# Kernel tuning notes

Measured on AMD Instinct MI355X. Metric: run time of the kernel, lower is better.

## Reference

```python
import jax, jax.numpy as jnp
import numpy as np

MID = 16
HEADS = 8
HEAD_DIM = MID // HEADS  # 2
EPS = 1e-5


def posembed(length, dim):
    # get_posembed_linear: sin-cos 1D positional embedding
    pos = jnp.arange(length, dtype=jnp.float32)
    omega = jnp.arange(dim // 2, dtype=jnp.float32) / (dim / 2.0)
    omega = 1.0 / (10000.0 ** omega)
    out = pos[:, None] * omega[None, :]  # [L, dim//2]
    return jnp.concatenate([jnp.sin(out), jnp.cos(out)], axis=1)  # [L, dim]


def layernorm(x, g, b):
    m = x.mean(-1, keepdims=True)
    v = ((x - m) ** 2).mean(-1, keepdims=True)
    return (x - m) * jax.lax.rsqrt(v + EPS) * g + b


def conv2d(x, w, b):
    # NCHW 3x3 SAME conv
    y = jax.lax.conv_general_dilated(x, w, (1, 1), 'SAME',
                                     dimension_numbers=('NCHW', 'OIHW', 'NCHW'))
    return y + b[None, :, None, None]


def attention(x, wq, wk, wv, wo, bo):
    # diffusers Attention: self-attn, no qkv bias, out bias
    B, S, C = x.shape
    q = (x @ wq.T).reshape(B, S, HEADS, HEAD_DIM)
    k = (x @ wk.T).reshape(B, S, HEADS, HEAD_DIM)
    v = (x @ wv.T).reshape(B, S, HEADS, HEAD_DIM)
    scale = 1.0 / np.sqrt(HEAD_DIM).astype(np.float32)
    scores = jnp.einsum('bshd,bthd->bhst', q, k) * scale
    p = jax.nn.softmax(scores, axis=-1)
    o = jnp.einsum('bhst,bthd->bshd', p, v).reshape(B, S, C)
    return o @ wo.T + bo


def setup_inputs() -> dict:
    key = jax.random.key(0)
    ks = jax.random.split(key, 24)

    def n(k, shape, s=0.05):
        return jax.random.normal(k, shape, dtype=jnp.float32) * s

    b, f, h, w, c = 2, 16, 64, 64, 16
    inp = {
        'hidden_states': n(ks[0], (b, f, h, w, c), 1.0),
        'ref_stats': n(ks[1], (b, f, h, w, c), 1.0),
        'emb': n(ks[2], (b, 512), 1.0),
        'conv_in_w': n(ks[3], (MID, c, 3, 3)),
        'conv_in_b': jnp.zeros((MID,), jnp.float32),
        'emb1_w': n(ks[4], (MID, 512)),
        'emb1_b': jnp.zeros((MID,), jnp.float32),
        'emb2_w': n(ks[5], (MID, MID)),
        'emb2_b': jnp.zeros((MID,), jnp.float32),
        'wqx': n(ks[6], (MID, MID)), 'wkx': n(ks[7], (MID, MID)),
        'wvx': n(ks[8], (MID, MID)), 'wox': n(ks[9], (MID, MID)),
        'box': jnp.zeros((MID,), jnp.float32),
        'wqy': n(ks[10], (MID, MID)), 'wky': n(ks[11], (MID, MID)),
        'wvy': n(ks[12], (MID, MID)), 'woy': n(ks[13], (MID, MID)),
        'boy': jnp.zeros((MID,), jnp.float32),
        'wqt': n(ks[14], (MID, MID)), 'wkt': n(ks[15], (MID, MID)),
        'wvt': n(ks[16], (MID, MID)), 'wot': n(ks[17], (MID, MID)),
        'bot': jnp.zeros((MID,), jnp.float32),
        'norm_g': jnp.ones((MID,), jnp.float32),
        'norm_b': jnp.zeros((MID,), jnp.float32),
        'proj_w': n(ks[18], (c, MID, 3, 3)),  # zero_module in torch; random here so grads flow
        'proj_b': jnp.zeros((c,), jnp.float32),
    }
    return inp


def reference(hidden_states, ref_stats, emb,
              conv_in_w, conv_in_b, emb1_w, emb1_b, emb2_w, emb2_b,
              wqx, wkx, wvx, wox, box,
              wqy, wky, wvy, woy, boy,
              wqt, wkt, wvt, wot, bot,
              norm_g, norm_b, proj_w, proj_b):
    b, f, h, w, c = hidden_states.shape

    # conv stem on (b f) c h w
    x = hidden_states.reshape(b * f, h, w, c).transpose(0, 3, 1, 2)
    x = conv2d(x, conv_in_w, conv_in_b)
    r = ref_stats.reshape(b * f, h, w, c).transpose(0, 3, 1, 2)
    r = conv2d(r, conv_in_w, conv_in_b)

    # TimestepEmbedding: linear -> silu -> linear, broadcast over frames/HW
    e = jax.nn.silu(emb @ emb1_w.T + emb1_b) @ emb2_w.T + emb2_b  # [b, MID]
    r = r + jnp.repeat(e, f, axis=0)[:, :, None, None]

    hs = x.reshape(b, f, MID, h, w).transpose(0, 1, 3, 4, 2)  # b f h w c
    rs = r.reshape(b, f, MID, h, w).transpose(0, 1, 3, 4, 2)

    # row (x) attention: cat along w -> (b f h) 2w c
    cat = jnp.concatenate([hs, rs], axis=3).reshape(b * f * h, 2 * w, MID)
    pe = posembed(2 * w, MID)
    resx = attention(layernorm(cat + pe[None], norm_g, norm_b), wqx, wkx, wvx, wox, box)
    resx = resx[:, :w].reshape(b, f, h, w, MID)

    # column (y) attention: cat along h -> (b f w) 2h c
    cat = jnp.concatenate([resx, rs], axis=2)            # b f 2h w c
    cat = cat.transpose(0, 1, 3, 2, 4).reshape(b * f * w, 2 * h, MID)
    pe = posembed(2 * h, MID)
    resy = attention(layernorm(cat + pe[None], norm_g, norm_b), wqy, wky, wvy, woy, boy)
    resy = resy[:, :h].reshape(b, f, w, h, MID).transpose(0, 1, 3, 2, 4)

    # temporal (t) attention: cat along f -> (b h w) 2f c
    cat = jnp.concatenate([resy, rs], axis=1)            # b 2f h w c
    cat = cat.transpose(0, 2, 3, 1, 4).reshape(b * h * w, 2 * f, MID)
    pe = posembed(2 * f, MID)
    rest = attention(layernorm(cat + pe[None], norm_g, norm_b), wqt, wkt, wvt, wot, bot)
    rest = rest[:, :f].reshape(b, h, w, f, MID).transpose(0, 3, 4, 1, 2).reshape(b * f, MID, h, w)

    out = conv2d(rest, proj_w, proj_b)  # (b f) c h w
    return hidden_states + out.reshape(b, f, c, h, w).transpose(0, 1, 3, 4, 2)
```

## Files before the change

kernel.cpp:

```cpp
#include <hip/hip_runtime.h>
#include <hip/hip_bf16.h>

typedef __hip_bfloat16 bf16;
using hf2 = decltype(__builtin_amdgcn_cvt_pkrtz(0.f, 0.f));
typedef float f32x2 __attribute__((ext_vector_type(2)));

__device__ __forceinline__ float b2f(bf16 x) { return __bfloat162float(x); }

#define BB   2
#define FF   16
#define HH   64
#define WW   64
#define CC   16
#define NIMG (BB*FF)
#define PIX  (HH*WW)
#define IMGSZ (PIX*CC)

#define QSCALE_LOG2E 1.0201394f

__device__ __forceinline__ unsigned pkh2(float a, float b) {
    union { hf2 h; unsigned u; } x;
    x.h = __builtin_amdgcn_cvt_pkrtz(a, b);
    return x.u;
}
__device__ __forceinline__ float fdot2u(unsigned a, unsigned b, float c) {
    union { unsigned u; hf2 h; } A, B;
    A.u = a; B.u = b;
    return __builtin_amdgcn_fdot2(A.h, B.h, c, false);
}
__device__ __forceinline__ f32x2 f2(float a, float b) {
    f32x2 r; r.x = a; r.y = b; return r;
}

__device__ __forceinline__ void ld16bf(const bf16* p, float* x) {
    const uint4* p4 = reinterpret_cast<const uint4*>(p);
    uint4 u0 = p4[0], u1 = p4[1];
    unsigned uu[8] = {u0.x, u0.y, u0.z, u0.w, u1.x, u1.y, u1.z, u1.w};
    #pragma unroll
    for (int k = 0; k < 8; ++k) {
        union { unsigned u; float f; } lo, hi;
        lo.u = uu[k] << 16;
        hi.u = uu[k] & 0xffff0000u;
        x[2 * k] = lo.f;
        x[2 * k + 1] = hi.f;
    }
}
__device__ __forceinline__ void st16bf(bf16* p, const float* x) {
    union { bf16 h[16]; uint4 u[2]; } o;
    #pragma unroll
    for (int k = 0; k < 16; ++k) o.h[k] = __float2bfloat16(x[k]);
    uint4* p4 = reinterpret_cast<uint4*>(p);
    p4[0] = o.u[0];
    p4[1] = o.u[1];
}

__device__ __forceinline__ void ld16f(const float* p, float* x) {
    const float4* p4 = reinterpret_cast<const float4*>(p);
    #pragma unroll
    for (int q = 0; q < 4; ++q) {
        float4 v = p4[q];
        x[4 * q] = v.x; x[4 * q + 1] = v.y; x[4 * q + 2] = v.z; x[4 * q + 3] = v.w;
    }
}
__device__ __forceinline__ void st16f(float* p, const float* x) {
    float4* p4 = reinterpret_cast<float4*>(p);
    #pragma unroll
    for (int q = 0; q < 4; ++q)
        p4[q] = make_float4(x[4 * q], x[4 * q + 1], x[4 * q + 2], x[4 * q + 3]);
}

__device__ __forceinline__ unsigned packbf2(float a, float b) {
    union { bf16 h[2]; unsigned u; } pk;
    pk.h[0] = __float2bfloat16(a);
    pk.h[1] = __float2bfloat16(b);
    return pk.u;
}

__global__ __launch_bounds__(256) void conv_in_kernel(
    const float* __restrict__ hid, const float* __restrict__ ref,
    const float* __restrict__ cw, const float* __restrict__ cb,
    const float* __restrict__ emb,
    const float* __restrict__ e1w, const float* __restrict__ e1b,
    const float* __restrict__ e2w, const float* __restrict__ e2b,
    bf16* __restrict__ A, bf16* __restrict__ R)
{
    __shared__ unsigned w2l[9 * 128];
    __shared__ float bl[16];
    __shared__ float hl[16];
    __shared__ float el[16];
    int t = threadIdx.x;
    if (t < 128) {
        int oc = t & 15, c2 = t >> 4;
        #pragma unroll
        for (int k = 0; k < 9; ++k)
            w2l[k * 128 + oc * 8 + c2] =
                pkh2(cw[(oc * 16 + 2 * c2) * 9 + k],
                     cw[(oc * 16 + 2 * c2 + 1) * 9 + k]);
    }
    if (t < 16) bl[t] = cb[t];

    int gid  = blockIdx.x * 256 + t;
    int wi   = gid & 63;
    int hi   = (gid >> 6) & 63;
    int img2 = gid >> 12;
    int isref = img2 >> 5;
    int img  = img2 & 31;
    int bi   = img >> 4;

    if (isref) {
        if (t < 16) {
            float acc = e1b[t];
            const float* er = emb + bi * 512;
            const float* wr = e1w + t * 512;
            for (int k = 0; k < 512; ++k) acc = fmaf(er[k], wr[k], acc);
            hl[t] = acc / (1.f + __expf(-acc));
        }
        __syncthreads();
        if (t < 16) {
            float acc = e2b[t];
            #pragma unroll
            for (int k = 0; k < 16; ++k) acc = fmaf(hl[k], e2w[t * 16 + k], acc);
            el[t] = acc;
        }
    }
    __syncthreads();

    const float* inp = (isref ? ref : hid) + (size_t)img * IMGSZ;
    float acc[16];
    #pragma unroll
    for (int oc = 0; oc < 16; ++oc)
        acc[oc] = bl[oc] + (isref ? el[oc] : 0.f);

    for (int ky = 0; ky < 3; ++ky) {
        int y = hi + ky - 1;
        if ((unsigned)y >= 64u) continue;
        for (int kx = 0; kx < 3; ++kx) {
            int x = wi + kx - 1;
            if ((unsigned)x >= 64u) continue;
            float xv[16];
            ld16f(inp + (((y << 6) + x) << 4), xv);
            unsigned xp[8];
            #pragma unroll
            for (int c2 = 0; c2 < 8; ++c2)
                xp[c2] = pkh2(xv[2 * c2], xv[2 * c2 + 1]);
            const unsigned* wt = &w2l[(ky * 3 + kx) * 128];
            #pragma unroll
            for (int oc = 0; oc < 16; ++oc) {
                float a = acc[oc];
                #pragma unroll
                for (int c2 = 0; c2 < 8; ++c2)
                    a = fdot2u(xp[c2], wt[oc * 8 + c2], a);
                acc[oc] = a;
            }
        }
    }
    bf16* op = (isref ? R : A) + ((size_t)(img * PIX + (hi << 6) + wi) << 4);
    st16bf(op, acc);
}

template<int S, int SEQPB, int MINW, bool F16OUT>
__global__ __launch_bounds__(256, MINW) void attn_kernel(
    bf16* __restrict__ A, const bf16* __restrict__ R,
    unsigned* __restrict__ A16,
    int d2, int str1, int str2, int tokStride,
    const float* __restrict__ wq, const float* __restrict__ wk,
    const float* __restrict__ wv, const float* __restrict__ wo,
    const float* __restrict__ bo, const float* __restrict__ gw,
    const float* __restrict__ bw)
{
    constexpr int HS  = S / 2;
    constexpr int KQ  = S / 2;
    constexpr int TPT = 256 / (SEQPB * S);
    constexpr int NDIM = 16 / TPT;
    constexpr int ITEMS = 256 / SEQPB;
    constexpr int NQG = ITEMS / 16;
    constexpr int QB  = HS / NQG;
    constexpr int QP  = QB / 2;
    constexpr int KROW = 10;
    constexpr int QROW = 20;
    constexpr int LSQ = (SEQPB == 1) ? 0 : ((SEQPB == 2) ? 1 : 2);
    constexpr int NW3 = SEQPB * HS * 8 / 256;

    __shared__ float wolT[256];
    __shared__ unsigned wq2L[128], wk2L[128], wv2L[128];
    __shared__ float bol[16], gl[16], blw[16];
    __shared__ __align__(16) unsigned kU[SEQPB * S * KROW];
    __shared__ __align__(16) unsigned vU[SEQPB * S * KROW];
    __shared__ __align__(16) unsigned qL[SEQPB * HS * KROW];
    __shared__ int bases[SEQPB];

    int t = threadIdx.x;
    wolT[(t & 15) * 16 + (t >> 4)] = wo[t];
    if (t < 128) {
        float2 qw = reinterpret_cast<const float2*>(wq)[t];
        float2 kw = reinterpret_cast<const float2*>(wk)[t];
        float2 vw = reinterpret_cast<const float2*>(wv)[t];
        wq2L[t] = pkh2(qw.x * QSCALE_LOG2E, qw.y * QSCALE_LOG2E);
        wk2L[t] = pkh2(kw.x, kw.y);
        wv2L[t] = pkh2(vw.x, vw.y);
    }
    if (t < 16) { bol[t] = bo[t]; gl[t] = gw[t]; blw[t] = bw[t]; }
    if (t < SEQPB) {
        int seq = blockIdx.x * SEQPB + t;
        bases[t] = (seq / d2) * str1 + (seq % d2) * str2;
    }
    __syncthreads();

    {
        int tokIdx = (TPT == 2) ? (t >> 1) : t;
        int db     = (TPT == 2) ? ((t & 1) * 8) : 0;
        int sq = tokIdx & (SEQPB - 1);
        int i  = tokIdx >> LSQ;
        const bf16* src = (i < HS)
            ? (A + bases[sq] + (size_t)i * tokStride)
            : (R + bases[sq] + (size_t)(i - HS) * tokStride);
        float x[16];
        ld16bf(src, x);
        const float om[8] = {1.f, 0.31622776601683794f, 0.1f, 0.031622776601683794f,
                             0.01f, 0.0031622776601683794f, 0.001f, 0.00031622776601683794f};
        float fi = (float)i;
        #pragma unroll
        for (int k = 0; k < 8; ++k) {
            float sv, cv;
            __sincosf(fi * om[k], &sv, &cv);
            x[k]     += sv;
            x[k + 8] += cv;
        }
        float m = 0.f;
        #pragma unroll
        for (int c = 0; c < 16; ++c) m += x[c];
        m *= (1.f / 16.f);
        float var = 0.f;
        #pragma unroll
        for (int c = 0; c < 16; ++c) { float d = x[c] - m; var = fmaf(d, d, var); }
        var *= (1.f / 16.f);
        float rs = rsqrtf(var + 1e-5f);
        float xn[16];
        #pragma unroll
        for (int c = 0; c < 16; ++c) xn[c] = (x[c] - m) * rs * gl[c] + blw[c];

        unsigned xp[8];
        #pragma unroll
        for (int c2 = 0; c2 < 8; ++c2) xp[c2] = pkh2(xn[2 * c2], xn[2 * c2 + 1]);

        float qv[NDIM], kv[NDIM], vv[NDIM];
        #pragma unroll
        for (int dd = 0; dd < NDIM; ++dd) {
            int d = db + dd;
            float aq = 0.f, ak = 0.f, av = 0.f;
            #pragma unroll
            for (int c2 = 0; c2 < 8; ++c2) {
                aq = fdot2u(xp[c2], wq2L[d * 8 + c2], aq);
                ak = fdot2u(xp[c2], wk2L[d * 8 + c2], ak);
                av = fdot2u(xp[c2], wv2L[d * 8 + c2], av);
            }
            qv[dd] = aq; kv[dd] = ak; vv[dd] = av;
        }
        int row = (sq * S + i) * KROW + (db >> 1);
        uint2* kr = reinterpret_cast<uint2*>(&kU[row]);
        uint2* vr = reinterpret_cast<uint2*>(&vU[row]);
        #pragma unroll
        for (int e = 0; e < NDIM / 4; ++e) {
            kr[e] = make_uint2(pkh2(kv[4 * e], kv[4 * e + 1]),
                               pkh2(kv[4 * e + 2], kv[4 * e + 3]));
            vr[e] = make_uint2(packbf2(vv[4 * e], vv[4 * e + 1]),
                               packbf2(vv[4 * e + 2], vv[4 * e + 3]));
        }
        if (i < HS) {
            uint2* qr = reinterpret_cast<uint2*>(&qL[(sq * HS + i) * KROW + (db >> 1)]);
            #pragma unroll
            for (int e = 0; e < NDIM / 4; ++e)
                qr[e] = make_uint2(pkh2(qv[4 * e], qv[4 * e + 1]),
                                   pkh2(qv[4 * e + 2], qv[4 * e + 3]));
        }
    }
    __syncthreads();

    int sq2 = t / ITEMS;
    int r   = t % ITEMS;
    int qg  = r >> 4;
    int hd  = (r >> 1) & 7;
    int half = r & 1;
    float* oL = reinterpret_cast<float*>(kU);
    {
        unsigned q2[QB];
        f32x2 l2[QP], a0p[QP], a1p[QP];
        #pragma unroll
        for (int qq = 0; qq < QB; ++qq)
            q2[qq] = qL[(sq2 * HS + qg * QB + qq) * KROW + hd];
        #pragma unroll
        for (int m = 0; m < QP; ++m) {
            l2[m] = f2(0.f, 0.f); a0p[m] = f2(0.f, 0.f); a1p[m] = f2(0.f, 0.f);
        }
        const unsigned* kp = &kU[(sq2 * S + half) * KROW + hd];
        const unsigned* vp = &vU[(sq2 * S + half) * KROW + hd];
        #pragma unroll 8
        for (int jj = 0; jj < KQ; ++jj) {
            unsigned ku = kp[jj * 2 * KROW];
            unsigned vu = vp[jj * 2 * KROW];
            union { unsigned u; float f; } v0, v1;
            v0.u = vu << 16; v1.u = vu & 0xffff0000u;
            f32x2 v00 = f2(v0.f, v0.f);
            f32x2 v11 = f2(v1.f, v1.f);
            #pragma unroll
            for (int m = 0; m < QP; ++m) {
                f32x2 p2;
                p2.x = __builtin_amdgcn_exp2f(fdot2u(q2[2 * m], ku, 0.f));
                p2.y = __builtin_amdgcn_exp2f(fdot2u(q2[2 * m + 1], ku, 0.f));
                l2[m] += p2;
                a0p[m] = __builtin_elementwise_fma(p2, v00, a0p[m]);
                a1p[m] = __builtin_elementwise_fma(p2, v11, a1p[m]);
            }
        }
        #pragma unroll
        for (int m = 0; m < QP; ++m) {
            l2[m].x  += __shfl_xor(l2[m].x, 1);  l2[m].y  += __shfl_xor(l2[m].y, 1);
            a0p[m].x += __shfl_xor(a0p[m].x, 1); a0p[m].y += __shfl_xor(a0p[m].y, 1);
            a1p[m].x += __shfl_xor(a1p[m].x, 1); a1p[m].y += __shfl_xor(a1p[m].y, 1);
        }
        __syncthreads();
        if (half == 0) {
            #pragma unroll
            for (int m = 0; m < QP; ++m) {
                float inv0 = 1.f / l2[m].x;
                float inv1 = 1.f / l2[m].y;
                *reinterpret_cast<float2*>(
                    &oL[(sq2 * HS + qg * QB + 2 * m) * QROW + 2 * hd]) =
                    make_float2(a0p[m].x * inv0, a1p[m].x * inv0);
                *reinterpret_cast<float2*>(
                    &oL[(sq2 * HS + qg * QB + 2 * m + 1) * QROW + 2 * hd]) =
                    make_float2(a0p[m].y * inv1, a1p[m].y * inv1);
            }
        }
    }
    __syncthreads();

    #pragma unroll
    for (int rep = 0; rep < NW3; ++rep) {
        int idx = t + rep * 256;
        int cp  = idx & 7;
        int g   = idx >> 3;
        int sq3 = g & (SEQPB - 1);
        int tok = g >> LSQ;
        const float* orow = &oL[(sq3 * HS + tok) * QROW];
        float acc0 = bol[2 * cp], acc1 = bol[2 * cp + 1];
        #pragma unroll
        for (int d = 0; d < 16; ++d) {
            acc0 = fmaf(orow[d], wolT[d * 16 + 2 * cp], acc0);
            acc1 = fmaf(orow[d], wolT[d * 16 + 2 * cp + 1], acc1);
        }
        int off = bases[sq3] + tok * tokStride;
        *reinterpret_cast<unsigned*>(A + off + 2 * cp) = packbf2(acc0, acc1);
        if constexpr (F16OUT)
            A16[(off >> 1) + cp] = pkh2(acc0, acc1);
    }
}

__global__ __launch_bounds__(256) void conv_out_kernel(
    const unsigned* __restrict__ A16, const float* __restrict__ hid,
    const float* __restrict__ pw, const float* __restrict__ pb,
    float* __restrict__ out)
{
    __shared__ unsigned w2l[9 * 128];
    __shared__ float bl[16];
    int t = threadIdx.x;
    if (t < 128) {
        int oc = t & 15, c2 = t >> 4;
        #pragma unroll
        for (int k = 0; k < 9; ++k)
            w2l[k * 128 + oc * 8 + c2] =
                pkh2(pw[(oc * 16 + 2 * c2) * 9 + k],
                     pw[(oc * 16 + 2 * c2 + 1) * 9 + k]);
    }
    if (t < 16) bl[t] = pb[t];
    __syncthreads();

    int gid = blockIdx.x * 256 + t;
    int wi = gid & 63, hi = (gid >> 6) & 63;
    int img = gid >> 12;
    const unsigned* inp = A16 + ((size_t)img << 15);
    float acc[16];
    #pragma unroll
    for (int oc = 0; oc < 16; ++oc) acc[oc] = bl[oc];

    for (int ky = 0; ky < 3; ++ky) {
        int y = hi + ky - 1;
        if ((unsigned)y >= 64u) continue;
        for (int kx = 0; kx < 3; ++kx) {
            int x = wi + kx - 1;
            if ((unsigned)x >= 64u) continue;
            const uint4* p4 = reinterpret_cast<const uint4*>(
                inp + (((y << 6) + x) << 3));
            uint4 u0 = p4[0], u1 = p4[1];
            unsigned xp[8] = {u0.x, u0.y, u0.z, u0.w, u1.x, u1.y, u1.z, u1.w};
            const unsigned* wt = &w2l[(ky * 3 + kx) * 128];
            #pragma unroll
            for (int oc = 0; oc < 16; ++oc) {
                float a = acc[oc];
                #pragma unroll
                for (int c2 = 0; c2 < 8; ++c2)
                    a = fdot2u(xp[c2], wt[oc * 8 + c2], a);
                acc[oc] = a;
            }
        }
    }
    size_t off = ((size_t)gid) << 4;
    float hv[16];
    ld16f(hid + off, hv);
    float res[16];
    #pragma unroll
    for (int k = 0; k < 16; ++k) res[k] = acc[k] + hv[k];
    st16f(out + off, res);
}

extern "C" void kernel_launch(void* const* d_in, const int* in_sizes, int n_in,
                              void* d_out, int out_size, void* d_ws, size_t ws_size,
                              hipStream_t stream) {
    const float* hid  = (const float*)d_in[0];
    const float* ref  = (const float*)d_in[1];
    const float* emb  = (const float*)d_in[2];
    const float* ciw  = (const float*)d_in[3];
    const float* cib  = (const float*)d_in[4];
    const float* e1w  = (const float*)d_in[5];
    const float* e1b  = (const float*)d_in[6];
    const float* e2w  = (const float*)d_in[7];
    const float* e2b  = (const float*)d_in[8];
    const float* wqx  = (const float*)d_in[9];
    const float* wkx  = (const float*)d_in[10];
    const float* wvx  = (const float*)d_in[11];
    const float* wox  = (const float*)d_in[12];
    const float* box_ = (const float*)d_in[13];
    const float* wqy  = (const float*)d_in[14];
    const float* wky  = (const float*)d_in[15];
    const float* wvy  = (const float*)d_in[16];
    const float* woy  = (const float*)d_in[17];
    const float* boy  = (const float*)d_in[18];
    const float* wqt  = (const float*)d_in[19];
    const float* wkt  = (const float*)d_in[20];
    const float* wvt  = (const float*)d_in[21];
    const float* wot  = (const float*)d_in[22];
    const float* bot  = (const float*)d_in[23];
    const float* ng   = (const float*)d_in[24];
    const float* nb   = (const float*)d_in[25];
    const float* pjw  = (const float*)d_in[26];
    const float* pjb  = (const float*)d_in[27];

    bf16* A = (bf16*)d_ws;
    unsigned* A16 = (unsigned*)((char*)d_ws + (4 << 20));
    bf16* R = (bf16*)d_out;

    conv_in_kernel<<<(2 * NIMG * PIX) / 256, 256, 0, stream>>>(
        hid, ref, ciw, cib, emb, e1w, e1b, e2w, e2b, A, R);

    attn_kernel<128, 1, 8, false><<<BB * FF * HH, 256, 0, stream>>>(
        A, R, nullptr, 1, WW * CC, 0, CC, wqx, wkx, wvx, wox, box_, ng, nb);
    attn_kernel<128, 2, 4, false><<<(BB * FF * WW) / 2, 256, 0, stream>>>(
        A, R, nullptr, WW, IMGSZ, CC, WW * CC, wqy, wky, wvy, woy, boy, ng, nb);
    attn_kernel<32, 4, 8, true><<<(BB * HH * WW) / 4, 256, 0, stream>>>(
        A, R, A16, HH * WW, FF * IMGSZ, CC, IMGSZ, wqt, wkt, wvt, wot, bot, ng, nb);

    conv_out_kernel<<<(NIMG * PIX) / 256, 256, 0, stream>>>(A16, hid, pjw, pjb, (float*)d_out);
}
```

Before: 243.1 us.

## Fuse input convolution with row (x) attention into one kernel

```diff
diff --git a/kernel.cpp b/kernel.cpp
--- a/kernel.cpp
+++ b/kernel.cpp
@@ -4,8 +4,6 @@
 typedef __hip_bfloat16 bf16;
 using hf2 = decltype(__builtin_amdgcn_cvt_pkrtz(0.f, 0.f));
 typedef float f32x2 __attribute__((ext_vector_type(2)));
-
-__device__ __forceinline__ float b2f(bf16 x) { return __bfloat162float(x); }
 
 #define BB   2
 #define FF   16
@@ -45,14 +43,6 @@
         x[2 * k + 1] = hi.f;
     }
 }
-__device__ __forceinline__ void st16bf(bf16* p, const float* x) {
-    union { bf16 h[16]; uint4 u[2]; } o;
-    #pragma unroll
-    for (int k = 0; k < 16; ++k) o.h[k] = __float2bfloat16(x[k]);
-    uint4* p4 = reinterpret_cast<uint4*>(p);
-    p4[0] = o.u[0];
-    p4[1] = o.u[1];
-}
 
 __device__ __forceinline__ void ld16f(const float* p, float* x) {
     const float4* p4 = reinterpret_cast<const float4*>(p);
@@ -76,20 +66,46 @@
     return pk.u;
 }
 
-__global__ __launch_bounds__(256) void conv_in_kernel(
+__global__ __launch_bounds__(256, 4) void convattn_x_kernel(
     const float* __restrict__ hid, const float* __restrict__ ref,
     const float* __restrict__ cw, const float* __restrict__ cb,
     const float* __restrict__ emb,
     const float* __restrict__ e1w, const float* __restrict__ e1b,
     const float* __restrict__ e2w, const float* __restrict__ e2b,
-    bf16* __restrict__ A, bf16* __restrict__ R)
+    bf16* __restrict__ A, bf16* __restrict__ R,
+    const float* __restrict__ wq, const float* __restrict__ wk,
+    const float* __restrict__ wv, const float* __restrict__ wo,
+    const float* __restrict__ bo, const float* __restrict__ gw,
+    const float* __restrict__ bw)
 {
+    constexpr int S = 128, HS = 64, KQ = 64;
+    constexpr int QB = 4, QP = 2;
+    constexpr int KROW = 10;
+    constexpr int QROW = 20;
+
     __shared__ unsigned w2l[9 * 128];
-    __shared__ float bl[16];
-    __shared__ float hl[16];
-    __shared__ float el[16];
+    __shared__ float wolT[256];
+    __shared__ unsigned wq2L[128], wk2L[128], wv2L[128];
+    __shared__ float bol[16], gl[16], blw[16], cbL[16], hl[16], el[16];
+    __shared__ __align__(16) unsigned kU[S * KROW];
+    __shared__ __align__(16) unsigned vU[S * KROW];
+    __shared__ __align__(16) unsigned qL[HS * KROW];
+
     int t = threadIdx.x;
+    int seq = blockIdx.x;
+    int h   = seq & 63;
+    int img = seq >> 6;
+    int b   = seq >> 10;
+    int base = img * IMGSZ + h * (WW * CC);
+
+    wolT[(t & 15) * 16 + (t >> 4)] = wo[t];
     if (t < 128) {
+        float2 qw = reinterpret_cast<const float2*>(wq)[t];
+        float2 kw = reinterpret_cast<const float2*>(wk)[t];
+        float2 vw = reinterpret_cast<const float2*>(wv)[t];
+        wq2L[t] = pkh2(qw.x * QSCALE_LOG2E, qw.y * QSCALE_LOG2E);
+        wk2L[t] = pkh2(kw.x, kw.y);
+        wv2L[t] = pkh2(vw.x, vw.y);
         int oc = t & 15, c2 = t >> 4;
         #pragma unroll
         for (int k = 0; k < 9; ++k)
@@ -97,65 +113,219 @@
                 pkh2(cw[(oc * 16 + 2 * c2) * 9 + k],
                      cw[(oc * 16 + 2 * c2 + 1) * 9 + k]);
     }
-    if (t < 16) bl[t] = cb[t];
-
-    int gid  = blockIdx.x * 256 + t;
-    int wi   = gid & 63;
-    int hi   = (gid >> 6) & 63;
-    int img2 = gid >> 12;
-    int isref = img2 >> 5;
-    int img  = img2 & 31;
-    int bi   = img >> 4;
-
-    if (isref) {
-        if (t < 16) {
-            float acc = e1b[t];
-            const float* er = emb + bi * 512;
-            const float* wr = e1w + t * 512;
-            for (int k = 0; k < 512; ++k) acc = fmaf(er[k], wr[k], acc);
-            hl[t] = acc / (1.f + __expf(-acc));
-        }
-        __syncthreads();
-        if (t < 16) {
-            float acc = e2b[t];
-            #pragma unroll
-            for (int k = 0; k < 16; ++k) acc = fmaf(hl[k], e2w[t * 16 + k], acc);
-            el[t] = acc;
-        }
-    }
-    __syncthreads();
-
-    const float* inp = (isref ? ref : hid) + (size_t)img * IMGSZ;
-    float acc[16];
-    #pragma unroll
-    for (int oc = 0; oc < 16; ++oc)
-        acc[oc] = bl[oc] + (isref ? el[oc] : 0.f);
-
-    for (int ky = 0; ky < 3; ++ky) {
-        int y = hi + ky - 1;
-        if ((unsigned)y >= 64u) continue;
-        for (int kx = 0; kx < 3; ++kx) {
-            int x = wi + kx - 1;
-            if ((unsigned)x >= 64u) continue;
-            float xv[16];
-            ld16f(inp + (((y << 6) + x) << 4), xv);
-            unsigned xp[8];
-            #pragma unroll
-            for (int c2 = 0; c2 < 8; ++c2)
-                xp[c2] = pkh2(xv[2 * c2], xv[2 * c2 + 1]);
-            const unsigned* wt = &w2l[(ky * 3 + kx) * 128];
-            #pragma unroll
-            for (int oc = 0; oc < 16; ++oc) {
-                float a = acc[oc];
+    if (t < 16) { bol[t] = bo[t]; gl[t] = gw[t]; blw[t] = bw[t]; cbL[t] = cb[t]; }
+
+    float* prt = reinterpret_cast<float*>(kU);
+    {
+        int o = t >> 4, seg = t & 15;
+        const float* er = emb + b * 512 + seg * 32;
+        const float* wr = e1w + o * 512 + seg * 32;
+        float p = 0.f;
+        #pragma unroll
+        for (int k = 0; k < 32; ++k) p = fmaf(er[k], wr[k], p);
+        prt[t] = p;
+    }
+    __syncthreads();
+    if (t < 16) {
+        float acc = e1b[t];
+        #pragma unroll
+        for (int s = 0; s < 16; ++s) acc += prt[t * 16 + s];
+        hl[t] = acc / (1.f + __expf(-acc));
+    }
+    __syncthreads();
+    if (t < 16) {
+        float acc = e2b[t];
+        #pragma unroll
+        for (int k = 0; k < 16; ++k) acc = fmaf(hl[k], e2w[t * 16 + k], acc);
+        el[t] = acc;
+    }
+    __syncthreads();
+
+    {
+        int i    = t >> 1;
+        int half = t & 1;
+        int db   = half * 8;
+        bool isR = (i >= HS);
+        int wi   = isR ? (i - HS) : i;
+        const float* src = (isR ? ref : hid) + (size_t)img * IMGSZ;
+
+        float x[8];
+        #pragma unroll
+        for (int k = 0; k < 8; ++k)
+            x[k] = cbL[db + k] + (isR ? el[db + k] : 0.f);
+
+        for (int ky = 0; ky < 3; ++ky) {
+            int y = h + ky - 1;
+            if ((unsigned)y >= 64u) continue;
+            for (int kx = 0; kx < 3; ++kx) {
+                int xx = wi + kx - 1;
+                if ((unsigned)xx >= 64u) continue;
+                float xv[16];
+                ld16f(src + (((y << 6) + xx) << 4), xv);
+                unsigned xpc[8];
                 #pragma unroll
                 for (int c2 = 0; c2 < 8; ++c2)
-                    a = fdot2u(xp[c2], wt[oc * 8 + c2], a);
-                acc[oc] = a;
-            }
-        }
-    }
-    bf16* op = (isref ? R : A) + ((size_t)(img * PIX + (hi << 6) + wi) << 4);
-    st16bf(op, acc);
+                    xpc[c2] = pkh2(xv[2 * c2], xv[2 * c2 + 1]);
+                const unsigned* wt = &w2l[(ky * 3 + kx) * 128];
+                #pragma unroll
+                for (int oo = 0; oo < 8; ++oo) {
+                    float a = x[oo];
+                    #pragma unroll
+                    for (int c2 = 0; c2 < 8; ++c2)
+                        a = fdot2u(xpc[c2], wt[(db + oo) * 8 + c2], a);
+                    x[oo] = a;
+                }
+            }
+        }
+
+        if (isR) {
+            union { unsigned u[4]; uint4 v; } rw;
+            #pragma unroll
+            for (int e = 0; e < 4; ++e)
+                rw.u[e] = packbf2(x[2 * e], x[2 * e + 1]);
+            *reinterpret_cast<uint4*>(R + base + wi * CC + db) = rw.v;
+        }
+
+        const float om[8] = {1.f, 0.31622776601683794f, 0.1f, 0.031622776601683794f,
+                             0.01f, 0.0031622776601683794f, 0.001f, 0.00031622776601683794f};
+        float fi = (float)i;
+        #pragma unroll
+        for (int k = 0; k < 8; ++k) {
+            float sv, cv;
+            __sincosf(fi * om[k], &sv, &cv);
+            x[k] += half ? cv : sv;
+        }
+
+        float s8 = 0.f;
+        #pragma unroll
+        for (int k = 0; k < 8; ++k) s8 += x[k];
+        float m = (s8 + __shfl_xor(s8, 1)) * (1.f / 16.f);
+        float v8 = 0.f;
+        #pragma unroll
+        for (int k = 0; k < 8; ++k) { float d = x[k] - m; v8 = fmaf(d, d, v8); }
+        float var = (v8 + __shfl_xor(v8, 1)) * (1.f / 16.f);
+        float rs = rsqrtf(var + 1e-5f);
+
+        unsigned xpm[4];
+        #pragma unroll
+        for (int e = 0; e < 4; ++e) {
+            float a0 = (x[2 * e]     - m) * rs * gl[db + 2 * e]     + blw[db + 2 * e];
+            float a1 = (x[2 * e + 1] - m) * rs * gl[db + 2 * e + 1] + blw[db + 2 * e + 1];
+            xpm[e] = pkh2(a0, a1);
+        }
+        unsigned xp[8];
+        #pragma unroll
+        for (int e = 0; e < 4; ++e) {
+            unsigned oth = __shfl_xor(xpm[e], 1);
+            xp[e]     = half ? oth    : xpm[e];
+            xp[e + 4] = half ? xpm[e] : oth;
+        }
+
+        float qv[8], kv[8], vv[8];
+        #pragma unroll
+        for (int dd = 0; dd < 8; ++dd) {
+            int d = db + dd;
+            float aq = 0.f, ak = 0.f, av = 0.f;
+            #pragma unroll
+            for (int c2 = 0; c2 < 8; ++c2) {
+                aq = fdot2u(xp[c2], wq2L[d * 8 + c2], aq);
+                ak = fdot2u(xp[c2], wk2L[d * 8 + c2], ak);
+                av = fdot2u(xp[c2], wv2L[d * 8 + c2], av);
+            }
+            qv[dd] = aq; kv[dd] = ak; vv[dd] = av;
+        }
+        int row = i * KROW + (db >> 1);
+        uint2* kr = reinterpret_cast<uint2*>(&kU[row]);
+        uint2* vr = reinterpret_cast<uint2*>(&vU[row]);
+        #pragma unroll
+        for (int e = 0; e < 2; ++e) {
+            kr[e] = make_uint2(pkh2(kv[4 * e], kv[4 * e + 1]),
+                               pkh2(kv[4 * e + 2], kv[4 * e + 3]));
+            vr[e] = make_uint2(packbf2(vv[4 * e], vv[4 * e + 1]),
+                               packbf2(vv[4 * e + 2], vv[4 * e + 3]));
+        }
+        if (i < HS) {
+            uint2* qr = reinterpret_cast<uint2*>(&qL[i * KROW + (db >> 1)]);
+            #pragma unroll
+            for (int e = 0; e < 2; ++e)
+                qr[e] = make_uint2(pkh2(qv[4 * e], qv[4 * e + 1]),
+                                   pkh2(qv[4 * e + 2], qv[4 * e + 3]));
+        }
+    }
+    __syncthreads();
+
+    int qg  = t >> 4;
+    int hd  = (t >> 1) & 7;
+    int half = t & 1;
+    float* oL = reinterpret_cast<float*>(kU);
+    {
+        unsigned q2[QB];
+        f32x2 l2[QP], a0p[QP], a1p[QP];
+        #pragma unroll
+        for (int qq = 0; qq < QB; ++qq)
+            q2[qq] = qL[(qg * QB + qq) * KROW + hd];
+        #pragma unroll
+        for (int m = 0; m < QP; ++m) {
+            l2[m] = f2(0.f, 0.f); a0p[m] = f2(0.f, 0.f); a1p[m] = f2(0.f, 0.f);
+        }
+        const unsigned* kp = &kU[half * KROW + hd];
+        const unsigned* vp = &vU[half * KROW + hd];
+        #pragma unroll 8
+        for (int jj = 0; jj < KQ; ++jj) {
+            unsigned ku = kp[jj * 2 * KROW];
+            unsigned vu = vp[jj * 2 * KROW];
+            union { unsigned u; float f; } v0, v1;
+            v0.u = vu << 16; v1.u = vu & 0xffff0000u;
+            f32x2 v00 = f2(v0.f, v0.f);
+            f32x2 v11 = f2(v1.f, v1.f);
+            #pragma unroll
+            for (int m = 0; m < QP; ++m) {
+                f32x2 p2;
+                p2.x = __builtin_amdgcn_exp2f(fdot2u(q2[2 * m], ku, 0.f));
+                p2.y = __builtin_amdgcn_exp2f(fdot2u(q2[2 * m + 1], ku, 0.f));
+                l2[m] += p2;
+                a0p[m] = __builtin_elementwise_fma(p2, v00, a0p[m]);
+                a1p[m] = __builtin_elementwise_fma(p2, v11, a1p[m]);
+            }
+        }
+        #pragma unroll
+        for (int m = 0; m < QP; ++m) {
+            l2[m].x  += __shfl_xor(l2[m].x, 1);  l2[m].y  += __shfl_xor(l2[m].y, 1);
+            a0p[m].x += __shfl_xor(a0p[m].x, 1); a0p[m].y += __shfl_xor(a0p[m].y, 1);
+            a1p[m].x += __shfl_xor(a1p[m].x, 1); a1p[m].y += __shfl_xor(a1p[m].y, 1);
+        }
+        __syncthreads();
+        if (half == 0) {
+            #pragma unroll
+            for (int m = 0; m < QP; ++m) {
+                float inv0 = 1.f / l2[m].x;
+                float inv1 = 1.f / l2[m].y;
+                *reinterpret_cast<float2*>(
+                    &oL[(qg * QB + 2 * m) * QROW + 2 * hd]) =
+                    make_float2(a0p[m].x * inv0, a1p[m].x * inv0);
+                *reinterpret_cast<float2*>(
+                    &oL[(qg * QB + 2 * m + 1) * QROW + 2 * hd]) =
+                    make_float2(a0p[m].y * inv1, a1p[m].y * inv1);
+            }
+        }
+    }
+    __syncthreads();
+
+    #pragma unroll
+    for (int rep = 0; rep < 2; ++rep) {
+        int idx = t + rep * 256;
+        int cp  = idx & 7;
+        int tok = idx >> 3;
+        const float* orow = &oL[tok * QROW];
+        float acc0 = bol[2 * cp], acc1 = bol[2 * cp + 1];
+        #pragma unroll
+        for (int d = 0; d < 16; ++d) {
+            acc0 = fmaf(orow[d], wolT[d * 16 + 2 * cp], acc0);
+            acc1 = fmaf(orow[d], wolT[d * 16 + 2 * cp + 1], acc1);
+        }
+        *reinterpret_cast<unsigned*>(A + base + tok * CC + 2 * cp) =
+            packbf2(acc0, acc1);
+    }
 }
 
 template<int S, int SEQPB, int MINW, bool F16OUT>
@@ -449,11 +619,10 @@
     unsigned* A16 = (unsigned*)((char*)d_ws + (4 << 20));
     bf16* R = (bf16*)d_out;
 
-    conv_in_kernel<<<(2 * NIMG * PIX) / 256, 256, 0, stream>>>(
-        hid, ref, ciw, cib, emb, e1w, e1b, e2w, e2b, A, R);
-
-    attn_kernel<128, 1, 8, false><<<BB * FF * HH, 256, 0, stream>>>(
-        A, R, nullptr, 1, WW * CC, 0, CC, wqx, wkx, wvx, wox, box_, ng, nb);
+    convattn_x_kernel<<<BB * FF * HH, 256, 0, stream>>>(
+        hid, ref, ciw, cib, emb, e1w, e1b, e2w, e2b,
+        A, R, wqx, wkx, wvx, wox, box_, ng, nb);
+
     attn_kernel<128, 2, 4, false><<<(BB * FF * WW) / 2, 256, 0, stream>>>(
         A, R, nullptr, WW, IMGSZ, CC, WW * CC, wqy, wky, wvy, woy, boy, ng, nb);
     attn_kernel<32, 4, 8, true><<<(BB * HH * WW) / 4, 256, 0, stream>>>(
```

Measured after the change: 251.0 us. 3.3% more time.

## Stage conv halo rows in LDS, parallelize emb reduction, split LN across thread pairs

Applied to the files above, without the earlier changes.

```diff
diff --git a/kernel.cpp b/kernel.cpp
--- a/kernel.cpp
+++ b/kernel.cpp
@@ -4,8 +4,6 @@
 typedef __hip_bfloat16 bf16;
 using hf2 = decltype(__builtin_amdgcn_cvt_pkrtz(0.f, 0.f));
 typedef float f32x2 __attribute__((ext_vector_type(2)));
-
-__device__ __forceinline__ float b2f(bf16 x) { return __bfloat162float(x); }
 
 #define BB   2
 #define FF   16
@@ -85,9 +83,9 @@
     bf16* __restrict__ A, bf16* __restrict__ R)
 {
     __shared__ unsigned w2l[9 * 128];
-    __shared__ float bl[16];
-    __shared__ float hl[16];
-    __shared__ float el[16];
+    __shared__ float bl[16], hl[16], el[16];
+    __shared__ __align__(16) unsigned stg[6 * 64 * 10];
+
     int t = threadIdx.x;
     if (t < 128) {
         int oc = t & 15, c2 = t >> 4;
@@ -102,17 +100,28 @@
     int gid  = blockIdx.x * 256 + t;
     int wi   = gid & 63;
     int hi   = (gid >> 6) & 63;
+    int r0   = hi & ~3;
     int img2 = gid >> 12;
     int isref = img2 >> 5;
     int img  = img2 & 31;
     int bi   = img >> 4;
 
     if (isref) {
+        float* red = reinterpret_cast<float*>(stg);
+        {
+            int o = t >> 4, seg = t & 15;
+            const float* er = emb + bi * 512 + seg * 32;
+            const float* wr = e1w + o * 512 + seg * 32;
+            float p = 0.f;
+            #pragma unroll
+            for (int k = 0; k < 32; ++k) p = fmaf(er[k], wr[k], p);
+            red[t] = p;
+        }
+        __syncthreads();
         if (t < 16) {
             float acc = e1b[t];
-            const float* er = emb + bi * 512;
-            const float* wr = e1w + t * 512;
-            for (int k = 0; k < 512; ++k) acc = fmaf(er[k], wr[k], acc);
+            #pragma unroll
+            for (int s = 0; s < 16; ++s) acc += red[t * 16 + s];
             hl[t] = acc / (1.f + __expf(-acc));
         }
         __syncthreads();
@@ -122,27 +131,47 @@
             for (int k = 0; k < 16; ++k) acc = fmaf(hl[k], e2w[t * 16 + k], acc);
             el[t] = acc;
         }
+        __syncthreads();
+    }
+
+    const float* inp = (isref ? ref : hid) + (size_t)img * IMGSZ;
+    #pragma unroll
+    for (int pass = 0; pass < 2; ++pass) {
+        int s = t + pass * 256;
+        if (s < 384) {
+            int px = s & 63, rr = s >> 6;
+            int y  = r0 - 1 + rr;
+            if ((unsigned)y < 64u) {
+                float xv[16];
+                ld16f(inp + (((y << 6) + px) << 4), xv);
+                uint2* dst = reinterpret_cast<uint2*>(&stg[(rr * 64 + px) * 10]);
+                #pragma unroll
+                for (int e = 0; e < 4; ++e)
+                    dst[e] = make_uint2(pkh2(xv[4 * e],     xv[4 * e + 1]),
+                                        pkh2(xv[4 * e + 2], xv[4 * e + 3]));
+            }
+        }
     }
     __syncthreads();
 
-    const float* inp = (isref ? ref : hid) + (size_t)img * IMGSZ;
+    int rb = hi & 3;
     float acc[16];
     #pragma unroll
     for (int oc = 0; oc < 16; ++oc)
         acc[oc] = bl[oc] + (isref ? el[oc] : 0.f);
 
+    #pragma unroll
     for (int ky = 0; ky < 3; ++ky) {
         int y = hi + ky - 1;
         if ((unsigned)y >= 64u) continue;
+        int rr = rb + ky;
+        #pragma unroll
         for (int kx = 0; kx < 3; ++kx) {
-            int x = wi + kx - 1;
-            if ((unsigned)x >= 64u) continue;
-            float xv[16];
-            ld16f(inp + (((y << 6) + x) << 4), xv);
-            unsigned xp[8];
-            #pragma unroll
-            for (int c2 = 0; c2 < 8; ++c2)
-                xp[c2] = pkh2(xv[2 * c2], xv[2 * c2 + 1]);
+            int xx = wi + kx - 1;
+            if ((unsigned)xx >= 64u) continue;
+            const uint2* pp = reinterpret_cast<const uint2*>(&stg[(rr * 64 + xx) * 10]);
+            uint2 p0 = pp[0], p1 = pp[1], p2 = pp[2], p3 = pp[3];
+            unsigned xp[8] = {p0.x, p0.y, p1.x, p1.y, p2.x, p2.y, p3.x, p3.y};
             const unsigned* wt = &w2l[(ky * 3 + kx) * 128];
             #pragma unroll
             for (int oc = 0; oc < 16; ++oc) {
@@ -171,7 +200,6 @@
     constexpr int HS  = S / 2;
     constexpr int KQ  = S / 2;
     constexpr int TPT = 256 / (SEQPB * S);
-    constexpr int NDIM = 16 / TPT;
     constexpr int ITEMS = 256 / SEQPB;
     constexpr int NQG = ITEMS / 16;
     constexpr int QB  = HS / NQG;
@@ -206,18 +234,96 @@
     }
     __syncthreads();
 
-    {
-        int tokIdx = (TPT == 2) ? (t >> 1) : t;
-        int db     = (TPT == 2) ? ((t & 1) * 8) : 0;
+    const float om[8] = {1.f, 0.31622776601683794f, 0.1f, 0.031622776601683794f,
+                         0.01f, 0.0031622776601683794f, 0.001f, 0.00031622776601683794f};
+
+    if constexpr (TPT == 2) {
+        int tokIdx = t >> 1;
+        int half = t & 1;
+        int db   = half * 8;
         int sq = tokIdx & (SEQPB - 1);
         int i  = tokIdx >> LSQ;
+        const bf16* src = ((i < HS)
+            ? (A + bases[sq] + (size_t)i * tokStride)
+            : (R + bases[sq] + (size_t)(i - HS) * tokStride)) + db;
+        uint4 u = *reinterpret_cast<const uint4*>(src);
+        unsigned uu[4] = {u.x, u.y, u.z, u.w};
+        float x[8];
+        #pragma unroll
+        for (int k = 0; k < 4; ++k) {
+            union { unsigned u; float f; } lo, hi2;
+            lo.u = uu[k] << 16; hi2.u = uu[k] & 0xffff0000u;
+            x[2 * k] = lo.f; x[2 * k + 1] = hi2.f;
+        }
+        float fi = (float)i;
+        #pragma unroll
+        for (int k = 0; k < 8; ++k) {
+            float sv, cv;
+            __sincosf(fi * om[k], &sv, &cv);
+            x[k] += half ? cv : sv;
+        }
+        float s8 = 0.f;
+        #pragma unroll
+        for (int k = 0; k < 8; ++k) s8 += x[k];
+        float m = (s8 + __shfl_xor(s8, 1)) * (1.f / 16.f);
+        float v8 = 0.f;
+        #pragma unroll
+        for (int k = 0; k < 8; ++k) { float d = x[k] - m; v8 = fmaf(d, d, v8); }
+        float var = (v8 + __shfl_xor(v8, 1)) * (1.f / 16.f);
+        float rs = rsqrtf(var + 1e-5f);
+
+        unsigned xpm[4];
+        #pragma unroll
+        for (int e = 0; e < 4; ++e) {
+            float a0 = (x[2 * e]     - m) * rs * gl[db + 2 * e]     + blw[db + 2 * e];
+            float a1 = (x[2 * e + 1] - m) * rs * gl[db + 2 * e + 1] + blw[db + 2 * e + 1];
+            xpm[e] = pkh2(a0, a1);
+        }
+        unsigned xp[8];
+        #pragma unroll
+        for (int e = 0; e < 4; ++e) {
+            unsigned oth = __shfl_xor(xpm[e], 1);
+            xp[e]     = half ? oth    : xpm[e];
+            xp[e + 4] = half ? xpm[e] : oth;
+        }
+        float qv[8], kv[8], vv[8];
+        #pragma unroll
+        for (int dd = 0; dd < 8; ++dd) {
+            int d = db + dd;
+            float aq = 0.f, ak = 0.f, av = 0.f;
+            #pragma unroll
+            for (int c2 = 0; c2 < 8; ++c2) {
+                aq = fdot2u(xp[c2], wq2L[d * 8 + c2], aq);
+                ak = fdot2u(xp[c2], wk2L[d * 8 + c2], ak);
+                av = fdot2u(xp[c2], wv2L[d * 8 + c2], av);
+            }
+            qv[dd] = aq; kv[dd] = ak; vv[dd] = av;
+        }
+        int row = (sq * S + i) * KROW + (db >> 1);
+        uint2* kr = reinterpret_cast<uint2*>(&kU[row]);
+        uint2* vr = reinterpret_cast<uint2*>(&vU[row]);
+        #pragma unroll
+        for (int e = 0; e < 2; ++e) {
+            kr[e] = make_uint2(pkh2(kv[4 * e], kv[4 * e + 1]),
+                               pkh2(kv[4 * e + 2], kv[4 * e + 3]));
+            vr[e] = make_uint2(packbf2(vv[4 * e], vv[4 * e + 1]),
+                               packbf2(vv[4 * e + 2], vv[4 * e + 3]));
+        }
+        if (i < HS) {
+            uint2* qr = reinterpret_cast<uint2*>(&qL[(sq * HS + i) * KROW + (db >> 1)]);
+            #pragma unroll
+            for (int e = 0; e < 2; ++e)
+                qr[e] = make_uint2(pkh2(qv[4 * e], qv[4 * e + 1]),
+                                   pkh2(qv[4 * e + 2], qv[4 * e + 3]));
+        }
+    } else {
+        int sq = t & (SEQPB - 1);
+        int i  = t >> LSQ;
         const bf16* src = (i < HS)
             ? (A + bases[sq] + (size_t)i * tokStride)
             : (R + bases[sq] + (size_t)(i - HS) * tokStride);
         float x[16];
         ld16bf(src, x);
-        const float om[8] = {1.f, 0.31622776601683794f, 0.1f, 0.031622776601683794f,
-                             0.01f, 0.0031622776601683794f, 0.001f, 0.00031622776601683794f};
         float fi = (float)i;
         #pragma unroll
         for (int k = 0; k < 8; ++k) {
@@ -243,33 +349,32 @@
         #pragma unroll
         for (int c2 = 0; c2 < 8; ++c2) xp[c2] = pkh2(xn[2 * c2], xn[2 * c2 + 1]);
 
-        float qv[NDIM], kv[NDIM], vv[NDIM];
-        #pragma unroll
-        for (int dd = 0; dd < NDIM; ++dd) {
-            int d = db + dd;
+        float qv[16], kv[16], vv[16];
+        #pragma unroll
+        for (int dd = 0; dd < 16; ++dd) {
             float aq = 0.f, ak = 0.f, av = 0.f;
             #pragma unroll
             for (int c2 = 0; c2 < 8; ++c2) {
-                aq = fdot2u(xp[c2], wq2L[d * 8 + c2], aq);
-                ak = fdot2u(xp[c2], wk2L[d * 8 + c2], ak);
-                av = fdot2u(xp[c2], wv2L[d * 8 + c2], av);
+                aq = fdot2u(xp[c2], wq2L[dd * 8 + c2], aq);
+                ak = fdot2u(xp[c2], wk2L[dd * 8 + c2], ak);
+                av = fdot2u(xp[c2], wv2L[dd * 8 + c2], av);
             }
             qv[dd] = aq; kv[dd] = ak; vv[dd] = av;
         }
-        int row = (sq * S + i) * KROW + (db >> 1);
+        int row = (sq * S + i) * KROW;
         uint2* kr = reinterpret_cast<uint2*>(&kU[row]);
         uint2* vr = reinterpret_cast<uint2*>(&vU[row]);
         #pragma unroll
-        for (int e = 0; e < NDIM / 4; ++e) {
+        for (int e = 0; e < 4; ++e) {
             kr[e] = make_uint2(pkh2(kv[4 * e], kv[4 * e + 1]),
                                pkh2(kv[4 * e + 2], kv[4 * e + 3]));
             vr[e] = make_uint2(packbf2(vv[4 * e], vv[4 * e + 1]),
                                packbf2(vv[4 * e + 2], vv[4 * e + 3]));
         }
         if (i < HS) {
-            uint2* qr = reinterpret_cast<uint2*>(&qL[(sq * HS + i) * KROW + (db >> 1)]);
-            #pragma unroll
-            for (int e = 0; e < NDIM / 4; ++e)
+            uint2* qr = reinterpret_cast<uint2*>(&qL[(sq * HS + i) * KROW]);
+            #pragma unroll
+            for (int e = 0; e < 4; ++e)
                 qr[e] = make_uint2(pkh2(qv[4 * e], qv[4 * e + 1]),
                                    pkh2(qv[4 * e + 2], qv[4 * e + 3]));
         }
@@ -280,7 +385,7 @@
     int r   = t % ITEMS;
     int qg  = r >> 4;
     int hd  = (r >> 1) & 7;
-    int half = r & 1;
+    int half2 = r & 1;
     float* oL = reinterpret_cast<float*>(kU);
     {
         unsigned q2[QB];
@@ -292,8 +397,8 @@
         for (int m = 0; m < QP; ++m) {
             l2[m] = f2(0.f, 0.f); a0p[m] = f2(0.f, 0.f); a1p[m] = f2(0.f, 0.f);
         }
-        const unsigned* kp = &kU[(sq2 * S + half) * KROW + hd];
-        const unsigned* vp = &vU[(sq2 * S + half) * KROW + hd];
+        const unsigned* kp = &kU[(sq2 * S + half2) * KROW + hd];
+        const unsigned* vp = &vU[(sq2 * S + half2) * KROW + hd];
         #pragma unroll 8
         for (int jj = 0; jj < KQ; ++jj) {
             unsigned ku = kp[jj * 2 * KROW];
@@ -319,7 +424,7 @@
             a1p[m].x += __shfl_xor(a1p[m].x, 1); a1p[m].y += __shfl_xor(a1p[m].y, 1);
         }
         __syncthreads();
-        if (half == 0) {
+        if (half2 == 0) {
             #pragma unroll
             for (int m = 0; m < QP; ++m) {
                 float inv0 = 1.f / l2[m].x;
@@ -363,6 +468,8 @@
 {
     __shared__ unsigned w2l[9 * 128];
     __shared__ float bl[16];
+    __shared__ __align__(16) unsigned stg[6 * 64 * 10];
+
     int t = threadIdx.x;
     if (t < 128) {
         int oc = t & 15, c2 = t >> 4;
@@ -373,26 +480,50 @@
                      pw[(oc * 16 + 2 * c2 + 1) * 9 + k]);
     }
     if (t < 16) bl[t] = pb[t];
-    __syncthreads();
 
     int gid = blockIdx.x * 256 + t;
     int wi = gid & 63, hi = (gid >> 6) & 63;
+    int r0 = hi & ~3;
     int img = gid >> 12;
     const unsigned* inp = A16 + ((size_t)img << 15);
+
+    #pragma unroll
+    for (int pass = 0; pass < 2; ++pass) {
+        int s = t + pass * 256;
+        if (s < 384) {
+            int px = s & 63, rr = s >> 6;
+            int y  = r0 - 1 + rr;
+            if ((unsigned)y < 64u) {
+                const uint4* sp = reinterpret_cast<const uint4*>(
+                    inp + (((y << 6) + px) << 3));
+                uint4 u0 = sp[0], u1 = sp[1];
+                uint2* dst = reinterpret_cast<uint2*>(&stg[(rr * 64 + px) * 10]);
+                dst[0] = make_uint2(u0.x, u0.y);
+                dst[1] = make_uint2(u0.z, u0.w);
+                dst[2] = make_uint2(u1.x, u1.y);
+                dst[3] = make_uint2(u1.z, u1.w);
+            }
+        }
+    }
+    __syncthreads();
+
+    int rb = hi & 3;
     float acc[16];
     #pragma unroll
     for (int oc = 0; oc < 16; ++oc) acc[oc] = bl[oc];
 
+    #pragma unroll
     for (int ky = 0; ky < 3; ++ky) {
         int y = hi + ky - 1;
         if ((unsigned)y >= 64u) continue;
+        int rr = rb + ky;
+        #pragma unroll
         for (int kx = 0; kx < 3; ++kx) {
-            int x = wi + kx - 1;
-            if ((unsigned)x >= 64u) continue;
-            const uint4* p4 = reinterpret_cast<const uint4*>(
-                inp + (((y << 6) + x) << 3));
-            uint4 u0 = p4[0], u1 = p4[1];
-            unsigned xp[8] = {u0.x, u0.y, u0.z, u0.w, u1.x, u1.y, u1.z, u1.w};
+            int xx = wi + kx - 1;
+            if ((unsigned)xx >= 64u) continue;
+            const uint2* pp = reinterpret_cast<const uint2*>(&stg[(rr * 64 + xx) * 10]);
+            uint2 p0 = pp[0], p1 = pp[1], p2 = pp[2], p3 = pp[3];
+            unsigned xp[8] = {p0.x, p0.y, p1.x, p1.y, p2.x, p2.y, p3.x, p3.y};
             const unsigned* wt = &w2l[(ky * 3 + kx) * 128];
             #pragma unroll
             for (int oc = 0; oc < 16; ++oc) {
```

Result: faster. 233.2 us (-4.1%).
